# Optimization experiments

Hardware: AMD Instinct MI355X
Metric: run time of the kernel (lower is better)

The kernel has to match this reference:

```python
import jax, jax.numpy as jnp
import numpy as np


def _dht(x):
    # Hartley transform via full fftn over ALL dims (matches torch dht2d(x, dim=None))
    f = jnp.fft.fftn(x)
    return f.real + f.imag


def setup_inputs() -> dict:
    key = jax.random.key(0)
    ks = jax.random.split(key, 5)
    B, H, W, C = 2, 128, 256, 768
    nb, fac = 8, 1
    bs = C // nb
    scale = 0.02
    x = jax.random.normal(ks[0], (B, H, W, C), dtype=jnp.float32)
    w1 = scale * jax.random.normal(ks[1], (2, nb, bs, bs * fac), dtype=jnp.float32)
    b1 = scale * jax.random.normal(ks[2], (2, nb, bs * fac), dtype=jnp.float32)
    w2 = scale * jax.random.normal(ks[3], (2, nb, bs * fac, bs), dtype=jnp.float32)
    b2 = scale * jax.random.normal(ks[4], (2, nb, bs), dtype=jnp.float32)
    return {"x": x, "w1": w1, "b1": b1, "w2": w2, "b2": b2}


def reference(x, w1, b1, w2, b2):
    SPARSITY = 0.01
    FRAC = 1.0  # hard_thresholding_fraction
    bias = x
    B, H, W, C = x.shape
    nb = w1.shape[1]
    bs = C // nb
    xf = x.astype(jnp.float32)

    X_k = _dht(xf).reshape(B, H, W, nb, bs)
    X_nk = jnp.roll(jnp.flip(xf, axis=(1, 2)), shift=(1, 1), axis=(1, 2)).reshape(B, H, W, nb, bs)

    total = H // 2 + 1
    kept = int(total * FRAC)
    r0, r1 = total - kept, min(total + kept, H)  # row slice clamps like torch slicing

    a = X_k[:, r0:r1, :kept]    # [B, Hs, kept, nb, bs]
    an = X_nk[:, r0:r1, :kept]

    ein = lambda t, w: jnp.einsum('bhwni,nio->bhwno', t, w)

    o1_k = jax.nn.relu(0.5 * (ein(a, w1[0]) - ein(an, w1[1]) + ein(a, w1[1]) + ein(an, w1[0])) + b1[0])
    o1_nk = jax.nn.relu(0.5 * (ein(an, w1[0]) - ein(a, w1[1]) + ein(an, w1[1]) + ein(a, w1[0])) + b1[1])

    o2_k = 0.5 * (ein(o1_k, w2[0]) - ein(o1_nk, w2[1]) + ein(o1_k, w2[1]) + ein(o1_nk, w2[0])) + b2[0]
    # NOTE: source genuinely uses o2_k (not o1_k) in two terms here; kept faithful.
    o2_nk = 0.5 * (ein(o1_nk, w2[0]) - ein(o2_k, w2[1]) + ein(o1_nk, w2[1]) + ein(o2_k, w2[0])) + b2[1]

    s = o2_k + o2_nk
    # softshrink
    s = jnp.sign(s) * jnp.maximum(jnp.abs(s) - SPARSITY, 0.0)

    full = jnp.zeros((B, H, W, nb, bs), jnp.float32).at[:, r0:r1, :kept].set(s)
    full = full.reshape(B, H, W, C)
    out = _dht(full) / full.size  # idht2d with dim=None: normalize by numel
    return out.astype(x.dtype) + bias
```

## Files before the change

kernel.cpp:

```cpp
#include <hip/hip_runtime.h>

#define BB 2
#define HH 128
#define WW 256
#define CC 768
#define NB 8
#define BS 96
#define WKEPT 65
#define NPTS (BB*HH*WKEPT)
#define NTOT ((size_t)BB*HH*WW*CC)
#define TWOPI 6.283185307179586f

#define P7_TW (16*65*8)

typedef __attribute__((ext_vector_type(8))) short bf16x8;
typedef __attribute__((ext_vector_type(4))) float f32x4;

__device__ __forceinline__ unsigned short f2bf(float f) {
    unsigned int u = __float_as_uint(f);
    u += 0x7fffu + ((u >> 16) & 1u);
    return (unsigned short)(u >> 16);
}
__device__ __forceinline__ float bf2f(unsigned short s) {
    return __uint_as_float((unsigned int)s << 16);
}

__global__ __launch_bounds__(256) void k_weights(
    const float* __restrict__ w1, const float* __restrict__ w2,
    const float* __restrict__ b2,
    unsigned short* __restrict__ W10h, unsigned short* __restrict__ W10l,
    unsigned short* __restrict__ W11h, unsigned short* __restrict__ W11l,
    unsigned short* __restrict__ WKPh, unsigned short* __restrict__ WKPl,
    unsigned short* __restrict__ WKMh, unsigned short* __restrict__ WKMl,
    float* __restrict__ BEFF)
{
    const int n = blockIdx.x;
    const int tid = threadIdx.x;
    __shared__ float m_s[BS*BS];

    const float* w2a = w2 + (size_t)(0*NB + n)*BS*BS;
    const float* w2b = w2 + (size_t)(1*NB + n)*BS*BS;
    for (int idx = tid; idx < BS*BS; idx += 256)
        m_s[idx] = 0.5f*(w2a[idx] - w2b[idx]);

    const float* w1a = w1 + (size_t)(0*NB + n)*BS*BS;
    const float* w1b = w1 + (size_t)(1*NB + n)*BS*BS;
    for (int idx = tid; idx < BS*BS; idx += 256) {
        int o = idx / BS, k = idx - o*BS;
        float v0 = w1a[k*BS + o];
        unsigned short h0 = f2bf(v0);
        unsigned short l0 = f2bf(v0 - bf2f(h0));
        W10h[n*BS*BS + idx] = h0;  W10l[n*BS*BS + idx] = l0;
        float v1 = w1b[k*BS + o];
        unsigned short h1 = f2bf(v1);
        unsigned short l1 = f2bf(v1 - bf2f(h1));
        W11h[n*BS*BS + idx] = h1;  W11l[n*BS*BS + idx] = l1;
    }
    __syncthreads();

    for (int idx = tid; idx < BS*BS; idx += 256) {
        int i = idx / BS, o = idx - i*BS;
        float p_io = 0.5f*(w2a[idx] + w2b[idx]);
        float m_io = m_s[idx];
        float accK = 0.f, accN = 0.f;
        for (int j = 0; j < BS; ++j) {
            float p_ij = 0.5f*(w2a[i*BS + j] + w2b[i*BS + j]);
            float mjo  = m_s[j*BS + o];
            accK += p_ij * mjo;
            accN += m_s[i*BS + j] * mjo;
        }
        float valK = p_io + accK;
        float valN = p_io + m_io + accN;
        float wkp = 0.5f*(valK + valN);
        float wkm = 0.5f*(valK - valN);
        int d = n*BS*BS + o*BS + i;
        unsigned short hp = f2bf(wkp);
        WKPh[d] = hp;  WKPl[d] = f2bf(wkp - bf2f(hp));
        unsigned short hm = f2bf(wkm);
        WKMh[d] = hm;  WKMl[d] = f2bf(wkm - bf2f(hm));
    }
    if (tid < BS) {
        const float* b2a = b2 + (0*NB + n)*BS;
        const float* b2b = b2 + (1*NB + n)*BS;
        float acc = b2a[tid] + b2b[tid];
        for (int j = 0; j < BS; ++j) acc += b2a[j] * m_s[j*BS + tid];
        BEFF[n*BS + tid] = acc;
    }
}

__global__ __launch_bounds__(256) void k_tw(
    float* __restrict__ c7t, float* __restrict__ s7t)
{
    int idx = blockIdx.x*256 + threadIdx.x;
    if (idx < P7_TW) {
        int j = idx & 7; int rest = idx >> 3;
        int wq = rest % 65; int wg = rest / 65;
        int ai = ((wg*8 + j) * wq) & 255;
        float sn, cs; sincosf(TWOPI * (float)ai / 256.0f, &sn, &cs);
        c7t[idx] = cs; s7t[idx] = sn;
    }
}

__global__ __launch_bounds__(256) void k_p1(
    const float* __restrict__ x, float2* __restrict__ out)
{
    const int tid = threadIdx.x;
    const int row = blockIdx.y;
    const int c0 = blockIdx.x * 16;
    __shared__ float2 tw[256];
    __shared__ float2 bufA[8*256];
    __shared__ float2 bufB[8*256];

    {
        float sn, cs; sincosf(TWOPI*(float)tid/256.f, &sn, &cs);
        tw[tid] = make_float2(cs, -sn);
    }
    const float* xr = x + (size_t)row * WW * CC + c0;
    for (int idx = tid; idx < 2048; idx += 256) {
        int l = idx & 7, w = idx >> 3;
        const float2 v = *(const float2*)(xr + (size_t)w*CC + 2*l);
        bufA[l*256 + w] = v;
    }
    __syncthreads();

    float2* src = bufA;
    float2* dst = bufB;
    const int t  = tid & 127;
    const int l0 = tid >> 7;
    #pragma unroll
    for (int st = 0; st < 8; ++st) {
        const int s = 1 << st;
        const int q = t & (s - 1);
        const int p = t >> st;
        const float2 w = tw[p << st];
        #pragma unroll
        for (int k = 0; k < 4; ++k) {
            int base = (l0 + 2*k) * 256;
            float2 a = src[base + q + s*p];
            float2 b = src[base + q + s*p + 128];
            float dx = a.x - b.x, dy = a.y - b.y;
            dst[base + q + 2*s*p]     = make_float2(a.x + b.x, a.y + b.y);
            dst[base + q + 2*s*p + s] = make_float2(dx*w.x - dy*w.y, dx*w.y + dy*w.x);
        }
        __syncthreads();
        float2* tmp = src; src = dst; dst = tmp;
    }
    for (int idx = tid; idx < 8*WKEPT; idx += 256) {
        int l = idx & 7, wp = idx >> 3;
        float2 Z  = src[l*256 + wp];
        float2 Zm = src[l*256 + ((256 - wp) & 255)];
        float2 U = make_float2(0.5f*(Z.x + Zm.x), 0.5f*(Z.y - Zm.y));
        float2 V = make_float2(0.5f*(Z.y + Zm.y), 0.5f*(Zm.x - Z.x));
        size_t g = (size_t)(row*WKEPT + wp)*CC + c0 + 2*l;
        out[g]     = U;
        out[g + 1] = V;
    }
}

#define LPB 4
__global__ __launch_bounds__(256) void k_cfft(
    const float2* __restrict__ in, float2* __restrict__ out)
{
    __shared__ float2 tw[CC];
    __shared__ float2 bufA[LPB*CC];
    __shared__ float2 bufB[LPB*CC];
    const int tid = threadIdx.x;
    const size_t line0 = (size_t)blockIdx.x * LPB;

    for (int t = tid; t < CC; t += 256) {
        float sn, cs; sincosf(TWOPI * (float)t / 768.0f, &sn, &cs);
        tw[t] = make_float2(cs, -sn);
    }
    for (int idx = tid; idx < LPB*CC; idx += 256) {
        int l = idx / CC, c = idx - l*CC;
        int m = c / 3, j = c - 3*m;
        bufA[l*CC + j*256 + m] = in[(line0 + l)*CC + c];
    }
    __syncthreads();

    float2* src = bufA;
    float2* dst = bufB;
    #pragma unroll
    for (int st = 0; st < 8; ++st) {
        const int s = 1 << st;
        const int h = 128 >> st;
        for (int item = tid; item < LPB*3*128; item += 256) {
            int sub = item >> 7;
            int t   = item & 127;
            int q = t & (s - 1);
            int p = t >> st;
            float2 a = src[sub*256 + q + s*p];
            float2 b = src[sub*256 + q + s*(p + h)];
            float2 w = tw[p * (3 << st)];
            float dx = a.x - b.x, dy = a.y - b.y;
            dst[sub*256 + q + s*(2*p)]     = make_float2(a.x + b.x, a.y + b.y);
            dst[sub*256 + q + s*(2*p + 1)] = make_float2(dx*w.x - dy*w.y, dx*w.y + dy*w.x);
        }
        __syncthreads();
        float2* tmp = src; src = dst; dst = tmp;
    }
    for (int idx = tid; idx < LPB*CC; idx += 256) {
        int l = idx / CC, cp = idx - l*CC;
        int r = cp & 255;
        float2 S0 = src[(l*3 + 0)*256 + r];
        float2 S1 = src[(l*3 + 1)*256 + r];
        float2 S2 = src[(l*3 + 2)*256 + r];
        float2 w1 = tw[cp];
        int i2 = 2*cp; if (i2 >= CC) i2 -= CC;
        float2 w2 = tw[i2];
        float fr = S0.x + w1.x*S1.x - w1.y*S1.y + w2.x*S2.x - w2.y*S2.y;
        float fi = S0.y + w1.x*S1.y + w1.y*S1.x + w2.x*S2.y + w2.y*S2.x;
        out[(line0 + l)*CC + cp] = make_float2(fr, fi);
    }
}

__global__ __launch_bounds__(256) void k_hb_c2a(
    const float2* __restrict__ in, float* __restrict__ aout)
{
    const int tid = threadIdx.x;
    const int wp = blockIdx.y;
    const int c0 = blockIdx.x * 8;
    __shared__ float2 tw[128];
    __shared__ float2 bufA[16*128];
    __shared__ float2 bufB[16*128];

    if (tid < 128) {
        float sn, cs; sincosf(TWOPI*(float)tid/128.f, &sn, &cs);
        tw[tid] = make_float2(cs, -sn);
    }
    for (int idx = tid; idx < 1024; idx += 256) {
        int cl = idx & 7, h = idx >> 3;
        float2 z0 = in[(size_t)((0*HH + h)*WKEPT + wp)*CC + c0 + cl];
        float2 z1 = in[(size_t)((1*HH + h)*WKEPT + wp)*CC + c0 + cl];
        bufA[(2*cl+0)*128 + h] = make_float2(z0.x+z1.x, z0.y+z1.y);
        bufA[(2*cl+1)*128 + h] = make_float2(z0.x-z1.x, z0.y-z1.y);
    }
    __syncthreads();

    float2* src = bufA;
    float2* dst = bufB;
    const int t  = tid & 63;
    const int l0 = tid >> 6;
    #pragma unroll
    for (int st = 0; st < 7; ++st) {
        const int s = 1 << st;
        const int q = t & (s - 1);
        const int p = t >> st;
        const float2 w = tw[p << st];
        #pragma unroll
        for (int k = 0; k < 4; ++k) {
            int base = (l0 + 4*k) * 128;
            float2 a = src[base + q + s*p];
            float2 b = src[base + q + s*p + 64];
            float dx = a.x - b.x, dy = a.y - b.y;
            dst[base + q + 2*s*p]     = make_float2(a.x + b.x, a.y + b.y);
            dst[base + q + 2*s*p + s] = make_float2(dx*w.x - dy*w.y, dx*w.y + dy*w.x);
        }
        __syncthreads();
        float2* tmp = src; src = dst; dst = tmp;
    }
    for (int idx = tid; idx < 2048; idx += 256) {
        int cl = idx & 7;
        int hp = (idx >> 3) & 127;
        int uv = idx >> 10;
        float2 z = src[(2*cl + uv)*128 + hp];
        aout[(size_t)((uv*HH + hp)*WKEPT + wp)*CC + c0 + cl] = z.x + z.y;
    }
}

__global__ __launch_bounds__(256) void k_hb_s2c(
    const float* __restrict__ sreal, float2* __restrict__ out)
{
    const int tid = threadIdx.x;
    const int wp = blockIdx.y;
    const int c0 = blockIdx.x * 16;
    __shared__ float2 tw[128];
    __shared__ float2 bufA[16*128];
    __shared__ float2 bufB[16*128];

    if (tid < 128) {
        float sn, cs; sincosf(TWOPI*(float)tid/128.f, &sn, &cs);
        tw[tid] = make_float2(cs, -sn);
    }
    for (int idx = tid; idx < 2048; idx += 256) {
        int cl = idx & 15, h = idx >> 4;
        float s0 = sreal[(size_t)((0*HH + h)*WKEPT + wp)*CC + c0 + cl];
        float s1 = sreal[(size_t)((1*HH + h)*WKEPT + wp)*CC + c0 + cl];
        bufA[cl*128 + h] = make_float2(s0 + s1, s0 - s1);
    }
    __syncthreads();

    float2* src = bufA;
    float2* dst = bufB;
    const int t  = tid & 63;
    const int l0 = tid >> 6;
    #pragma unroll
    for (int st = 0; st < 7; ++st) {
        const int s = 1 << st;
        const int q = t & (s - 1);
        const int p = t >> st;
        const float2 w = tw[p << st];
        #pragma unroll
        for (int k = 0; k < 4; ++k) {
            int base = (l0 + 4*k) * 128;
            float2 a = src[base + q + s*p];
            float2 b = src[base + q + s*p + 64];
            float dx = a.x - b.x, dy = a.y - b.y;
            dst[base + q + 2*s*p]     = make_float2(a.x + b.x, a.y + b.y);
            dst[base + q + 2*s*p + s] = make_float2(dx*w.x - dy*w.y, dx*w.y + dy*w.x);
        }
        __syncthreads();
        float2* tmp = src; src = dst; dst = tmp;
    }
    for (int idx = tid; idx < 2048; idx += 256) {
        int cl = idx & 15;
        int hp = idx >> 4;
        float2 A  = src[cl*128 + hp];
        float2 Zm = src[cl*128 + ((128 - hp) & 127)];
        float2 U = make_float2(0.5f*(A.x + Zm.x), 0.5f*(A.y - Zm.y));
        float2 V = make_float2(0.5f*(A.y + Zm.y), 0.5f*(Zm.x - A.x));
        out[(size_t)((0*HH + hp)*WKEPT + wp)*CC + c0 + cl] = U;
        out[(size_t)((1*HH + hp)*WKEPT + wp)*CC + c0 + cl] = V;
    }
}

__global__ __launch_bounds__(256, 2) void k_mlp(
    const float* __restrict__ a, const float* __restrict__ x,
    const unsigned short* __restrict__ W10h, const unsigned short* __restrict__ W10l,
    const unsigned short* __restrict__ W11h, const unsigned short* __restrict__ W11l,
    const unsigned short* __restrict__ WKPh, const unsigned short* __restrict__ WKPl,
    const unsigned short* __restrict__ WKMh, const unsigned short* __restrict__ WKMl,
    const float* __restrict__ b1, const float* __restrict__ BEFF,
    float* __restrict__ sout)
{
    const int tid = threadIdx.x;
    const int n = blockIdx.y;
    const int P0 = blockIdx.x * 64;
    __shared__ unsigned short Wh_A[96*48], Wl_A[96*48];
    __shared__ unsigned short Wh_B[96*48], Wl_B[96*48];
    __shared__ unsigned short PMp[64*104], PMm[64*104];

    const int lane = tid & 63;
    const int wv = tid >> 6;
    const int lr = lane & 15;
    const int lk = lane >> 4;

    const int Pld = P0 + 16*wv + lr;
    int bb = Pld / (HH*WKEPT);
    int rem = Pld - bb*(HH*WKEPT);
    int h = rem / WKEPT;
    int wq = rem - h*WKEPT;
    int hh2 = (HH - h) & (HH-1);
    int ww2 = (WW - wq) & (WW-1);
    const float* aRow  = a + (size_t)Pld*CC + n*BS;
    const float* anRow = x + (size_t)((bb*HH + hh2)*WW + ww2)*CC + n*BS;

    f32x4 T1[6], T2[6];
    #pragma unroll
    for (int t = 0; t < 6; ++t) {
        T1[t] = (f32x4){0.f,0.f,0.f,0.f};
        T2[t] = (f32x4){0.f,0.f,0.f,0.f};
    }

    for (int ks = 0; ks < 3; ++ks) {
        __syncthreads();
        for (int idx = tid; idx < 96*16; idx += 256) {
            int o = idx >> 4, kp = (idx & 15) << 1;
            int g = n*BS*BS + o*BS + ks*32 + kp;
            *(ushort2*)&Wh_A[o*48 + kp] = *(const ushort2*)&W10h[g];
            *(ushort2*)&Wl_A[o*48 + kp] = *(const ushort2*)&W10l[g];
            *(ushort2*)&Wh_B[o*48 + kp] = *(const ushort2*)&W11h[g];
            *(ushort2*)&Wl_B[o*48 + kp] = *(const ushort2*)&W11l[g];
        }
        __syncthreads();

        const int kseg = ks*32 + 8*lk;
        float4 a0 = *(const float4*)(aRow + kseg);
        float4 a1 = *(const float4*)(aRow + kseg + 4);
        float4 n0 = *(const float4*)(anRow + kseg);
        float4 n1 = *(const float4*)(anRow + kseg + 4);
        bf16x8 uF, vF;
        uF[0] = (short)f2bf(0.5f*(a0.x + n0.x));  vF[0] = (short)f2bf(0.5f*(a0.x - n0.x));
        uF[1] = (short)f2bf(0.5f*(a0.y + n0.y));  vF[1] = (short)f2bf(0.5f*(a0.y - n0.y));
        uF[2] = (short)f2bf(0.5f*(a0.z + n0.z));  vF[2] = (short)f2bf(0.5f*(a0.z - n0.z));
        uF[3] = (short)f2bf(0.5f*(a0.w + n0.w));  vF[3] = (short)f2bf(0.5f*(a0.w - n0.w));
        uF[4] = (short)f2bf(0.5f*(a1.x + n1.x));  vF[4] = (short)f2bf(0.5f*(a1.x - n1.x));
        uF[5] = (short)f2bf(0.5f*(a1.y + n1.y));  vF[5] = (short)f2bf(0.5f*(a1.y - n1.y));
        uF[6] = (short)f2bf(0.5f*(a1.z + n1.z));  vF[6] = (short)f2bf(0.5f*(a1.z - n1.z));
        uF[7] = (short)f2bf(0.5f*(a1.w + n1.w));  vF[7] = (short)f2bf(0.5f*(a1.w - n1.w));

        #pragma unroll
        for (int t = 0; t < 6; ++t) {
            int wb = (16*t + lr)*48 + 8*lk;
            bf16x8 bh = *(const bf16x8*)&Wh_A[wb];
            T1[t] = __builtin_amdgcn_mfma_f32_16x16x32_bf16(uF, bh, T1[t], 0, 0, 0);
            bf16x8 bl = *(const bf16x8*)&Wl_A[wb];
            T1[t] = __builtin_amdgcn_mfma_f32_16x16x32_bf16(uF, bl, T1[t], 0, 0, 0);
            bf16x8 ch = *(const bf16x8*)&Wh_B[wb];
            T2[t] = __builtin_amdgcn_mfma_f32_16x16x32_bf16(vF, ch, T2[t], 0, 0, 0);
            bf16x8 cl = *(const bf16x8*)&Wl_B[wb];
            T2[t] = __builtin_amdgcn_mfma_f32_16x16x32_bf16(vF, cl, T2[t], 0, 0, 0);
        }
    }

    #pragma unroll
    for (int t = 0; t < 6; ++t) {
        float bk = b1[(0*NB + n)*BS + 16*t + lr];
        float bn = b1[(1*NB + n)*BS + 16*t + lr];
        #pragma unroll
        for (int r = 0; r < 4; ++r) {
            float ok = fmaxf(T1[t][r] + T2[t][r] + bk, 0.f);
            float on = fmaxf(T1[t][r] - T2[t][r] + bn, 0.f);
            int pl = 16*wv + 4*lk + r;
            PMp[pl*104 + 16*t + lr] = f2bf(ok + on);
            PMm[pl*104 + 16*t + lr] = f2bf(ok - on);
        }
    }

    f32x4 S[6];
    #pragma unroll
    for (int t = 0; t < 6; ++t) S[t] = (f32x4){0.f,0.f,0.f,0.f};
    for (int ks = 0; ks < 3; ++ks) {
        __syncthreads();
        for (int idx = tid; idx < 96*16; idx += 256) {
            int o = idx >> 4, kp = (idx & 15) << 1;
            int g = n*BS*BS + o*BS + ks*32 + kp;
            *(ushort2*)&Wh_A[o*48 + kp] = *(const ushort2*)&WKPh[g];
            *(ushort2*)&Wl_A[o*48 + kp] = *(const ushort2*)&WKPl[g];
            *(ushort2*)&Wh_B[o*48 + kp] = *(const ushort2*)&WKMh[g];
            *(ushort2*)&Wl_B[o*48 + kp] = *(const ushort2*)&WKMl[g];
        }
        __syncthreads();

        const int kseg = ks*32 + 8*lk;
        bf16x8 pF = *(const bf16x8*)&PMp[(16*wv + lr)*104 + kseg];
        bf16x8 mF = *(const bf16x8*)&PMm[(16*wv + lr)*104 + kseg];
        #pragma unroll
        for (int t = 0; t < 6; ++t) {
            int wb = (16*t + lr)*48 + 8*lk;
            bf16x8 bh = *(const bf16x8*)&Wh_A[wb];
            S[t] = __builtin_amdgcn_mfma_f32_16x16x32_bf16(pF, bh, S[t], 0, 0, 0);
            bf16x8 bl = *(const bf16x8*)&Wl_A[wb];
            S[t] = __builtin_amdgcn_mfma_f32_16x16x32_bf16(pF, bl, S[t], 0, 0, 0);
            bf16x8 ch = *(const bf16x8*)&Wh_B[wb];
            S[t] = __builtin_amdgcn_mfma_f32_16x16x32_bf16(mF, ch, S[t], 0, 0, 0);
            bf16x8 cl = *(const bf16x8*)&Wl_B[wb];
            S[t] = __builtin_amdgcn_mfma_f32_16x16x32_bf16(mF, cl, S[t], 0, 0, 0);
        }
    }

    #pragma unroll
    for (int t = 0; t < 6; ++t) {
        float be = BEFF[n*BS + 16*t + lr];
        #pragma unroll
        for (int r = 0; r < 4; ++r) {
            float v = S[t][r] + be;
            float av2 = fabsf(v) - 0.01f;
            float sv = (av2 > 0.f) ? copysignf(av2, v) : 0.f;
            int pt = P0 + 16*wv + 4*lk + r;
            sout[(size_t)pt*CC + n*BS + 16*t + lr] = sv;
        }
    }
}

__global__ __launch_bounds__(256) void k_p7(
    const float2* __restrict__ A, const float* __restrict__ x,
    const float* __restrict__ c7t, const float* __restrict__ s7t,
    float* __restrict__ out)
{
    const int tid = threadIdx.x;
    const int ct = blockIdx.x % 3;
    const int wg = blockIdx.x / 3;
    const int rg = blockIdx.y;
    const int c  = ct*256 + tid;
    const int wpb = wg*8;
    const int row0 = rg*4;

    float accA[4][8], accB[4][8], acc128[4];
    #pragma unroll
    for (int r = 0; r < 4; ++r) {
        acc128[r] = 0.f;
        #pragma unroll
        for (int j = 0; j < 8; ++j) { accA[r][j] = 0.f; accB[r][j] = 0.f; }
    }

    const float2* A0 = A + (size_t)row0 * WKEPT * CC + c;
    const float4* cT = (const float4*)(c7t + (size_t)wg*65*8);
    const float4* sT = (const float4*)(s7t + (size_t)wg*65*8);
    for (int wq = 0; wq < 65; ++wq) {
        float4 c0 = cT[2*wq], c1 = cT[2*wq+1];
        float4 s0 = sT[2*wq], s1 = sT[2*wq+1];
        float sg = (wq & 1) ? -1.f : 1.f;
        #pragma unroll
        for (int r = 0; r < 4; ++r) {
            float2 v = A0[(size_t)(r*WKEPT + wq) * CC];
            float P = v.x + v.y;
            float M = v.y - v.x;
            float N = v.x - v.y;
            acc128[r] = fmaf(sg, P, acc128[r]);
            accA[r][0] = fmaf(P, c0.x, fmaf(M, s0.x, accA[r][0]));
            accB[r][0] = fmaf(P, c0.x, fmaf(N, s0.x, accB[r][0]));
            accA[r][1] = fmaf(P, c0.y, fmaf(M, s0.y, accA[r][1]));
            accB[r][1] = fmaf(P, c0.y, fmaf(N, s0.y, accB[r][1]));
            accA[r][2] = fmaf(P, c0.z, fmaf(M, s0.z, accA[r][2]));
            accB[r][2] = fmaf(P, c0.z, fmaf(N, s0.z, accB[r][2]));
            accA[r][3] = fmaf(P, c0.w, fmaf(M, s0.w, accA[r][3]));
            accB[r][3] = fmaf(P, c0.w, fmaf(N, s0.w, accB[r][3]));
            accA[r][4] = fmaf(P, c1.x, fmaf(M, s1.x, accA[r][4]));
            accB[r][4] = fmaf(P, c1.x, fmaf(N, s1.x, accB[r][4]));
            accA[r][5] = fmaf(P, c1.y, fmaf(M, s1.y, accA[r][5]));
            accB[r][5] = fmaf(P, c1.y, fmaf(N, s1.y, accB[r][5]));
            accA[r][6] = fmaf(P, c1.z, fmaf(M, s1.z, accA[r][6]));
            accB[r][6] = fmaf(P, c1.z, fmaf(N, s1.z, accB[r][6]));
            accA[r][7] = fmaf(P, c1.w, fmaf(M, s1.w, accA[r][7]));
            accB[r][7] = fmaf(P, c1.w, fmaf(N, s1.w, accB[r][7]));
        }
    }

    const float scale = 1.0f / 50331648.0f;
    #pragma unroll
    for (int r = 0; r < 4; ++r) {
        size_t base = (size_t)(row0 + r) * WW * CC + c;
        #pragma unroll
        for (int j = 0; j < 8; ++j) {
            int w = wpb + j;
            size_t g = base + (size_t)w*CC;
            out[g] = fmaf(accA[r][j], scale, x[g]);
            if (w != 0) {
                size_t g2 = base + (size_t)(256 - w)*CC;
                out[g2] = fmaf(accB[r][j], scale, x[g2]);
            }
        }
        if (wg == 0) {
            size_t g = base + (size_t)128*CC;
            out[g] = fmaf(acc128[r], scale, x[g]);
        }
    }
}

__global__ __launch_bounds__(256) void k_p7_fb(
    const float2* __restrict__ A, const float* __restrict__ x,
    float* __restrict__ out)
{
    const int tid = threadIdx.x;
    const int ct = blockIdx.x % 3;
    const int wg = blockIdx.x / 3;
    const int h = blockIdx.y, b = blockIdx.z;
    const int c = ct*256 + tid;
    __shared__ float cm[WKEPT][8];
    __shared__ float cp[WKEPT][8];
    for (int idx = tid; idx < WKEPT*8; idx += 256) {
        int wq = idx >> 3, j = idx & 7;
        int w = wg*8 + j;
        int ai = (w * wq) & 255;
        float sn, cse; sincosf(TWOPI * (float)ai / 256.f, &sn, &cse);
        cm[wq][j] = cse - sn;
        cp[wq][j] = cse + sn;
    }
    __syncthreads();
    float acc[8] = {0,0,0,0,0,0,0,0};
    const float2* Ab = A + (size_t)((b*HH + h)*WKEPT)*CC + c;
    for (int wq = 0; wq < WKEPT; ++wq) {
        float2 v = Ab[(size_t)wq*CC];
        const float4* m4 = (const float4*)(&cm[wq][0]);
        const float4* p4 = (const float4*)(&cp[wq][0]);
        #pragma unroll
        for (int jj = 0; jj < 2; ++jj) {
            float4 qm = m4[jj], qp = p4[jj];
            acc[4*jj+0] += v.x*qm.x + v.y*qp.x;
            acc[4*jj+1] += v.x*qm.y + v.y*qp.y;
            acc[4*jj+2] += v.x*qm.z + v.y*qp.z;
            acc[4*jj+3] += v.x*qm.w + v.y*qp.w;
        }
    }
    const float scale = 1.0f / 50331648.0f;
    size_t base = (size_t)(b*HH + h)*WW*CC + c;
    #pragma unroll
    for (int j = 0; j < 8; ++j) {
        int w = wg*8 + j;
        size_t g = base + (size_t)w*CC;
        out[g] = fmaf(acc[j], scale, x[g]);
    }
}

extern "C" void kernel_launch(void* const* d_in, const int* in_sizes, int n_in,
                              void* d_out, int out_size, void* d_ws, size_t ws_size,
                              hipStream_t stream)
{
    (void)in_sizes; (void)n_in; (void)out_size;
    const float* x  = (const float*)d_in[0];
    const float* w1 = (const float*)d_in[1];
    const float* b1 = (const float*)d_in[2];
    const float* w2 = (const float*)d_in[3];
    const float* b2 = (const float*)d_in[4];

    float*  ws     = (float*)d_ws;
    float2* Abuf   = (float2*)d_ws;
    float*  a_real = ws;
    float*  s_real = ws + (size_t)NPTS*CC;
    float*  BEFF   = ws + 2*(size_t)NPTS*CC;
    float*  c7t    = BEFF + NB*BS;
    float*  s7t    = c7t + P7_TW;
    unsigned short* Wq = (unsigned short*)(s7t + P7_TW);
    const size_t WSZ = (size_t)NB*BS*BS;
    unsigned short* W10h = Wq + 0*WSZ;
    unsigned short* W10l = Wq + 1*WSZ;
    unsigned short* W11h = Wq + 2*WSZ;
    unsigned short* W11l = Wq + 3*WSZ;
    unsigned short* WKPh = Wq + 4*WSZ;
    unsigned short* WKPl = Wq + 5*WSZ;
    unsigned short* WKMh = Wq + 6*WSZ;
    unsigned short* WKMl = Wq + 7*WSZ;

    const size_t need_bytes =
        ((size_t)2*NPTS*CC + NB*BS + 2*P7_TW)*4 + 8*WSZ*2;
    const bool fast = (ws_size >= need_bytes);

    float2* Bc   = (float2*)d_out;
    float*  outf = (float*)d_out;

    k_weights<<<dim3(NB), dim3(256), 0, stream>>>(
        w1, w2, b2, W10h, W10l, W11h, W11l, WKPh, WKPl, WKMh, WKMl, BEFF);
    if (fast) {
        k_tw<<<dim3(33), dim3(256), 0, stream>>>(c7t, s7t);
    }
    k_p1     <<<dim3(48, 256), dim3(256), 0, stream>>>(x, Abuf);
    k_cfft   <<<dim3(NPTS/LPB), dim3(256), 0, stream>>>(Abuf, Bc);
    k_hb_c2a <<<dim3(96, WKEPT), dim3(256), 0, stream>>>(Bc, a_real);
    k_mlp    <<<dim3(260, NB), dim3(256), 0, stream>>>(
        a_real, x, W10h, W10l, W11h, W11l, WKPh, WKPl, WKMh, WKMl,
        b1, BEFF, s_real);
    k_hb_s2c <<<dim3(48, WKEPT), dim3(256), 0, stream>>>(s_real, Bc);
    k_cfft   <<<dim3(NPTS/LPB), dim3(256), 0, stream>>>(Bc, Abuf);
    if (fast) {
        k_p7<<<dim3(48, 64), dim3(256), 0, stream>>>(Abuf, x, c7t, s7t, outf);
    } else {
        k_p7_fb<<<dim3(96, HH, BB), dim3(256), 0, stream>>>(Abuf, x, outf);
    }
}
```

Measured before the change: 1.086 ms.

## Replace direct-DFT final W pass with shared-memory radix-2 Stockham FFT

The final pass previously did a direct 65-to-256 point DFT using precomputed twiddle tables. It now runs a zero-padded 256-point radix-2 Stockham FFT in shared memory for 8 channels per block. This cuts arithmetic and removes the twiddle-table kernel and its fallback path. In exchange, global loads and stores cover only 8 contiguous channels (32–64 byte segments), which hurts coalescing, and the FFT adds 8 block-wide barriers per stage sequence.

New measurement: 1.146 ms. 1.05x slower.

```diff
diff --git a/kernel.cpp b/kernel.cpp
--- a/kernel.cpp
+++ b/kernel.cpp
@@ -10,8 +10,6 @@
 #define NPTS (BB*HH*WKEPT)
 #define NTOT ((size_t)BB*HH*WW*CC)
 #define TWOPI 6.283185307179586f
-
-#define P7_TW (16*65*8)
 
 typedef __attribute__((ext_vector_type(8))) short bf16x8;
 typedef __attribute__((ext_vector_type(4))) float f32x4;
@@ -85,19 +83,6 @@
         float acc = b2a[tid] + b2b[tid];
         for (int j = 0; j < BS; ++j) acc += b2a[j] * m_s[j*BS + tid];
         BEFF[n*BS + tid] = acc;
-    }
-}
-
-__global__ __launch_bounds__(256) void k_tw(
-    float* __restrict__ c7t, float* __restrict__ s7t)
-{
-    int idx = blockIdx.x*256 + threadIdx.x;
-    if (idx < P7_TW) {
-        int j = idx & 7; int rest = idx >> 3;
-        int wq = rest % 65; int wg = rest / 65;
-        int ai = ((wg*8 + j) * wq) & 255;
-        float sn, cs; sincosf(TWOPI * (float)ai / 256.0f, &sn, &cs);
-        c7t[idx] = cs; s7t[idx] = sn;
     }
 }
 
@@ -465,121 +450,56 @@
 
 __global__ __launch_bounds__(256) void k_p7(
     const float2* __restrict__ A, const float* __restrict__ x,
-    const float* __restrict__ c7t, const float* __restrict__ s7t,
     float* __restrict__ out)
 {
     const int tid = threadIdx.x;
-    const int ct = blockIdx.x % 3;
-    const int wg = blockIdx.x / 3;
-    const int rg = blockIdx.y;
-    const int c  = ct*256 + tid;
-    const int wpb = wg*8;
-    const int row0 = rg*4;
-
-    float accA[4][8], accB[4][8], acc128[4];
-    #pragma unroll
-    for (int r = 0; r < 4; ++r) {
-        acc128[r] = 0.f;
-        #pragma unroll
-        for (int j = 0; j < 8; ++j) { accA[r][j] = 0.f; accB[r][j] = 0.f; }
-    }
-
-    const float2* A0 = A + (size_t)row0 * WKEPT * CC + c;
-    const float4* cT = (const float4*)(c7t + (size_t)wg*65*8);
-    const float4* sT = (const float4*)(s7t + (size_t)wg*65*8);
-    for (int wq = 0; wq < 65; ++wq) {
-        float4 c0 = cT[2*wq], c1 = cT[2*wq+1];
-        float4 s0 = sT[2*wq], s1 = sT[2*wq+1];
-        float sg = (wq & 1) ? -1.f : 1.f;
-        #pragma unroll
-        for (int r = 0; r < 4; ++r) {
-            float2 v = A0[(size_t)(r*WKEPT + wq) * CC];
-            float P = v.x + v.y;
-            float M = v.y - v.x;
-            float N = v.x - v.y;
-            acc128[r] = fmaf(sg, P, acc128[r]);
-            accA[r][0] = fmaf(P, c0.x, fmaf(M, s0.x, accA[r][0]));
-            accB[r][0] = fmaf(P, c0.x, fmaf(N, s0.x, accB[r][0]));
-            accA[r][1] = fmaf(P, c0.y, fmaf(M, s0.y, accA[r][1]));
-            accB[r][1] = fmaf(P, c0.y, fmaf(N, s0.y, accB[r][1]));
-            accA[r][2] = fmaf(P, c0.z, fmaf(M, s0.z, accA[r][2]));
-            accB[r][2] = fmaf(P, c0.z, fmaf(N, s0.z, accB[r][2]));
-            accA[r][3] = fmaf(P, c0.w, fmaf(M, s0.w, accA[r][3]));
-            accB[r][3] = fmaf(P, c0.w, fmaf(N, s0.w, accB[r][3]));
-            accA[r][4] = fmaf(P, c1.x, fmaf(M, s1.x, accA[r][4]));
-            accB[r][4] = fmaf(P, c1.x, fmaf(N, s1.x, accB[r][4]));
-            accA[r][5] = fmaf(P, c1.y, fmaf(M, s1.y, accA[r][5]));
-            accB[r][5] = fmaf(P, c1.y, fmaf(N, s1.y, accB[r][5]));
-            accA[r][6] = fmaf(P, c1.z, fmaf(M, s1.z, accA[r][6]));
-            accB[r][6] = fmaf(P, c1.z, fmaf(N, s1.z, accB[r][6]));
-            accA[r][7] = fmaf(P, c1.w, fmaf(M, s1.w, accA[r][7]));
-            accB[r][7] = fmaf(P, c1.w, fmaf(N, s1.w, accB[r][7]));
-        }
-    }
-
+    const int row = blockIdx.y;
+    const int c0 = blockIdx.x * 8;
+    __shared__ float2 tw[256];
+    __shared__ float2 bufA[8*256];
+    __shared__ float2 bufB[8*256];
+
+    {
+        float sn, cs; sincosf(TWOPI*(float)tid/256.f, &sn, &cs);
+        tw[tid] = make_float2(cs, -sn);
+    }
+    const float2* Ar = A + (size_t)row * WKEPT * CC + c0;
+    for (int idx = tid; idx < 2048; idx += 256) {
+        int l = idx & 7, w = idx >> 3;
+        bufA[l*256 + w] = (w < WKEPT) ? Ar[(size_t)w*CC + l]
+                                      : make_float2(0.f, 0.f);
+    }
+    __syncthreads();
+
+    float2* src = bufA;
+    float2* dst = bufB;
+    const int t  = tid & 127;
+    const int l0 = tid >> 7;
+    #pragma unroll
+    for (int st = 0; st < 8; ++st) {
+        const int s = 1 << st;
+        const int q = t & (s - 1);
+        const int p = t >> st;
+        const float2 w = tw[p << st];
+        #pragma unroll
+        for (int k = 0; k < 4; ++k) {
+            int base = (l0 + 2*k) * 256;
+            float2 a = src[base + q + s*p];
+            float2 b = src[base + q + s*p + 128];
+            float dx = a.x - b.x, dy = a.y - b.y;
+            dst[base + q + 2*s*p]     = make_float2(a.x + b.x, a.y + b.y);
+            dst[base + q + 2*s*p + s] = make_float2(dx*w.x - dy*w.y, dx*w.y + dy*w.x);
+        }
+        __syncthreads();
+        float2* tmp = src; src = dst; dst = tmp;
+    }
     const float scale = 1.0f / 50331648.0f;
-    #pragma unroll
-    for (int r = 0; r < 4; ++r) {
-        size_t base = (size_t)(row0 + r) * WW * CC + c;
-        #pragma unroll
-        for (int j = 0; j < 8; ++j) {
-            int w = wpb + j;
-            size_t g = base + (size_t)w*CC;
-            out[g] = fmaf(accA[r][j], scale, x[g]);
-            if (w != 0) {
-                size_t g2 = base + (size_t)(256 - w)*CC;
-                out[g2] = fmaf(accB[r][j], scale, x[g2]);
-            }
-        }
-        if (wg == 0) {
-            size_t g = base + (size_t)128*CC;
-            out[g] = fmaf(acc128[r], scale, x[g]);
-        }
-    }
-}
-
-__global__ __launch_bounds__(256) void k_p7_fb(
-    const float2* __restrict__ A, const float* __restrict__ x,
-    float* __restrict__ out)
-{
-    const int tid = threadIdx.x;
-    const int ct = blockIdx.x % 3;
-    const int wg = blockIdx.x / 3;
-    const int h = blockIdx.y, b = blockIdx.z;
-    const int c = ct*256 + tid;
-    __shared__ float cm[WKEPT][8];
-    __shared__ float cp[WKEPT][8];
-    for (int idx = tid; idx < WKEPT*8; idx += 256) {
-        int wq = idx >> 3, j = idx & 7;
-        int w = wg*8 + j;
-        int ai = (w * wq) & 255;
-        float sn, cse; sincosf(TWOPI * (float)ai / 256.f, &sn, &cse);
-        cm[wq][j] = cse - sn;
-        cp[wq][j] = cse + sn;
-    }
-    __syncthreads();
-    float acc[8] = {0,0,0,0,0,0,0,0};
-    const float2* Ab = A + (size_t)((b*HH + h)*WKEPT)*CC + c;
-    for (int wq = 0; wq < WKEPT; ++wq) {
-        float2 v = Ab[(size_t)wq*CC];
-        const float4* m4 = (const float4*)(&cm[wq][0]);
-        const float4* p4 = (const float4*)(&cp[wq][0]);
-        #pragma unroll
-        for (int jj = 0; jj < 2; ++jj) {
-            float4 qm = m4[jj], qp = p4[jj];
-            acc[4*jj+0] += v.x*qm.x + v.y*qp.x;
-            acc[4*jj+1] += v.x*qm.y + v.y*qp.y;
-            acc[4*jj+2] += v.x*qm.z + v.y*qp.z;
-            acc[4*jj+3] += v.x*qm.w + v.y*qp.w;
-        }
-    }
-    const float scale = 1.0f / 50331648.0f;
-    size_t base = (size_t)(b*HH + h)*WW*CC + c;
-    #pragma unroll
-    for (int j = 0; j < 8; ++j) {
-        int w = wg*8 + j;
-        size_t g = base + (size_t)w*CC;
-        out[g] = fmaf(acc[j], scale, x[g]);
+    const size_t obase = (size_t)row * WW * CC + c0;
+    for (int idx = tid; idx < 2048; idx += 256) {
+        int l = idx & 7, w = idx >> 3;
+        float2 z = src[l*256 + w];
+        size_t g = obase + (size_t)w*CC + l;
+        out[g] = fmaf(z.x + z.y, scale, x[g]);
     }
 }
 
@@ -587,7 +507,7 @@
                               void* d_out, int out_size, void* d_ws, size_t ws_size,
                               hipStream_t stream)
 {
-    (void)in_sizes; (void)n_in; (void)out_size;
+    (void)in_sizes; (void)n_in; (void)out_size; (void)ws_size;
     const float* x  = (const float*)d_in[0];
     const float* w1 = (const float*)d_in[1];
     const float* b1 = (const float*)d_in[2];
@@ -599,9 +519,7 @@
     float*  a_real = ws;
     float*  s_real = ws + (size_t)NPTS*CC;
     float*  BEFF   = ws + 2*(size_t)NPTS*CC;
-    float*  c7t    = BEFF + NB*BS;
-    float*  s7t    = c7t + P7_TW;
-    unsigned short* Wq = (unsigned short*)(s7t + P7_TW);
+    unsigned short* Wq = (unsigned short*)(BEFF + NB*BS);
     const size_t WSZ = (size_t)NB*BS*BS;
     unsigned short* W10h = Wq + 0*WSZ;
     unsigned short* W10l = Wq + 1*WSZ;
@@ -612,18 +530,11 @@
     unsigned short* WKMh = Wq + 6*WSZ;
     unsigned short* WKMl = Wq + 7*WSZ;
 
-    const size_t need_bytes =
-        ((size_t)2*NPTS*CC + NB*BS + 2*P7_TW)*4 + 8*WSZ*2;
-    const bool fast = (ws_size >= need_bytes);
-
     float2* Bc   = (float2*)d_out;
     float*  outf = (float*)d_out;
 
     k_weights<<<dim3(NB), dim3(256), 0, stream>>>(
         w1, w2, b2, W10h, W10l, W11h, W11l, WKPh, WKPl, WKMh, WKMl, BEFF);
-    if (fast) {
-        k_tw<<<dim3(33), dim3(256), 0, stream>>>(c7t, s7t);
-    }
     k_p1     <<<dim3(48, 256), dim3(256), 0, stream>>>(x, Abuf);
     k_cfft   <<<dim3(NPTS/LPB), dim3(256), 0, stream>>>(Abuf, Bc);
     k_hb_c2a <<<dim3(96, WKEPT), dim3(256), 0, stream>>>(Bc, a_real);
@@ -632,9 +543,5 @@
         b1, BEFF, s_real);
     k_hb_s2c <<<dim3(48, WKEPT), dim3(256), 0, stream>>>(s_real, Bc);
     k_cfft   <<<dim3(NPTS/LPB), dim3(256), 0, stream>>>(Bc, Abuf);
-    if (fast) {
-        k_p7<<<dim3(48, 64), dim3(256), 0, stream>>>(Abuf, x, c7t, s7t, outf);
-    } else {
-        k_p7_fb<<<dim3(96, HH, BB), dim3(256), 0, stream>>>(Abuf, x, outf);
-    }
-}
+    k_p7     <<<dim3(96, 256), dim3(256), 0, stream>>>(Abuf, x, outf);
+}
```
